# Kernel optimization log

Measured on AMD Instinct MI355X. Metric: run time of the kernel, lower is better.

## Reference

```python
import jax, jax.numpy as jnp
import numpy as np

DIM, HEADS, HD, WS, SHIFT = 768, 48, 16, 3, 1
EPS = 1e-5


def setup_inputs() -> dict:
    key = jax.random.key(0)
    ks = jax.random.split(key, 6)
    s = 0.02  # init scale for weights
    return {
        "x": jax.random.normal(ks[0], (8, 4096, DIM), jnp.float32),
        "g1": jnp.ones((DIM,), jnp.float32),
        "b1": jnp.zeros((DIM,), jnp.float32),
        "w_qkv": jax.random.normal(ks[1], (DIM, 3 * DIM), jnp.float32) * s,
        "w_proj": jax.random.normal(ks[2], (DIM, DIM), jnp.float32) * s,
        "g2": jnp.ones((DIM,), jnp.float32),
        "b2": jnp.zeros((DIM,), jnp.float32),
        "w_mlp1": jax.random.normal(ks[3], (DIM, 2 * DIM), jnp.float32) * s,
        "b_mlp1": jnp.zeros((2 * DIM,), jnp.float32),
        "w_mlp2": jax.random.normal(ks[4], (2 * DIM, DIM), jnp.float32) * s,
        "b_mlp2": jnp.zeros((DIM,), jnp.float32),
    }


def _ln(x, g, b):
    m = x.mean(-1, keepdims=True)
    v = ((x - m) ** 2).mean(-1, keepdims=True)
    return (x - m) * jax.lax.rsqrt(v + EPS) * g + b


def _shifted_window_attention(x, w_qkv, w_proj):
    B, T, C = x.shape
    pad_r = (WS - T % WS) % WS
    xp = jnp.pad(x, ((0, 0), (0, pad_r), (0, 0)))
    Tp = T + pad_r
    xs = jnp.roll(xp, -SHIFT, axis=1) if SHIFT > 0 else xp
    xw = xs.reshape(B, Tp // WS, WS, C)            # [B, nW, ws, C]
    qkv = (xw @ w_qkv).reshape(B, Tp // WS, WS, 3, HEADS, HD)
    q, k, v = jnp.moveaxis(qkv, 3, 0)              # each [B, nW, ws, H, hd]
    attn = jnp.einsum("bnihd,bnjhd->bnhij", q, k) * (HD ** -0.5)
    attn = jax.nn.softmax(attn, axis=-1)           # [B, nW, H, ws, ws]
    o = jnp.einsum("bnhij,bnjhd->bnihd", attn, v).reshape(B, Tp, C)
    o = o @ w_proj
    if SHIFT > 0:
        o = jnp.roll(o, SHIFT, axis=1)
    return o[:, :T]


def reference(x, g1, b1, w_qkv, w_proj, g2, b2, w_mlp1, b_mlp1, w_mlp2, b_mlp2):
    x = x + _shifted_window_attention(_ln(x, g1, b1), w_qkv, w_proj)
    h = _ln(x, g2, b2)
    x = x + (jax.nn.relu(h @ w_mlp1 + b_mlp1) @ w_mlp2 + b_mlp2)
    return x
```

## Files before the change

kernel.cpp:

```cpp
#include <hip/hip_runtime.h>

#define BATCH 8
#define TLEN  4096
#define DIM   768
#define TP    4098
#define NWIN  1366
#define HEADS 48
#define HD    16
#define MREAL (BATCH*TP)
#define MP    32896
#define M2    (BATCH*TLEN)

typedef unsigned short u16;
typedef __bf16  bf16x8  __attribute__((ext_vector_type(8)));
typedef short   short8v __attribute__((ext_vector_type(8)));
typedef float   float4v __attribute__((ext_vector_type(4)));
typedef u16     u16x4   __attribute__((ext_vector_type(4)));

static __device__ __forceinline__ float bf2f(u16 u) {
  unsigned int x = ((unsigned int)u) << 16;
  return __builtin_bit_cast(float, x);
}
static __device__ __forceinline__ u16 f2bf(float f) {
  unsigned int x = __builtin_bit_cast(unsigned int, f);
  x += 0x7fffu + ((x >> 16) & 1u);
  return (u16)(x >> 16);
}

static __device__ __forceinline__ float4v mfma_bf16(short8v a, short8v b, float4v c) {
  return __builtin_amdgcn_mfma_f32_16x16x32_bf16(
      __builtin_bit_cast(bf16x8, a), __builtin_bit_cast(bf16x8, b), c, 0, 0, 0);
}

static __device__ __forceinline__ void gload_lds16(const u16* src, u16* ldsdst) {
  __builtin_amdgcn_global_load_lds(
      (const __attribute__((address_space(1))) void*)src,
      (__attribute__((address_space(3))) void*)ldsdst,
      16, 0, 0);
}

__global__ __launch_bounds__(256) void cvt_transpose(const float* __restrict__ w,
                                                     u16* __restrict__ wt,
                                                     int K, int N) {
  int idx = blockIdx.x * 256 + threadIdx.x;
  if (idx >= K * N) return;
  int k = idx / N, n = idx - k * N;
  wt[(size_t)n * K + k] = f2bf(w[idx]);
}

template<bool ROLL>
__global__ __launch_bounds__(256) void ln_kernel(const float* __restrict__ x,
                                                 const float* __restrict__ g,
                                                 const float* __restrict__ bet,
                                                 u16* __restrict__ out) {
  int wave = threadIdx.x >> 6, lane = threadIdx.x & 63;
  int row = blockIdx.x * 4 + wave;
  u16* orow = out + (size_t)row * DIM;

  const float* src;
  if (ROLL) {
    bool zero = (row >= MREAL);
    int t = 0, b = 0;
    if (!zero) {
      b = row / TP;
      int m = row - b * TP;
      t = m + 1; if (t == TP) t = 0;
      if (t >= TLEN) zero = true;
    }
    if (zero) {
      u16x4 z = {};
#pragma unroll
      for (int c = 0; c < 3; ++c) *(u16x4*)&orow[c * 256 + lane * 4] = z;
      return;
    }
    src = x + ((size_t)b * TLEN + t) * DIM;
  } else {
    src = x + (size_t)row * DIM;
  }

  float v[12];
  float s = 0.f, s2 = 0.f;
#pragma unroll
  for (int c = 0; c < 3; ++c) {
    float4v f = *(const float4v*)&src[c * 256 + lane * 4];
#pragma unroll
    for (int q = 0; q < 4; ++q) { v[c * 4 + q] = f[q]; s += f[q]; s2 += f[q] * f[q]; }
  }
#pragma unroll
  for (int off = 1; off < 64; off <<= 1) {
    s  += __shfl_xor(s, off);
    s2 += __shfl_xor(s2, off);
  }
  float mean = s * (1.f / DIM);
  float var  = s2 * (1.f / DIM) - mean * mean;
  float rs   = rsqrtf(var + 1e-5f);
#pragma unroll
  for (int c = 0; c < 3; ++c) {
    int col = c * 256 + lane * 4;
    float4v gv = *(const float4v*)&g[col];
    float4v bv = *(const float4v*)&bet[col];
    u16x4 o4;
#pragma unroll
    for (int q = 0; q < 4; ++q) o4[q] = f2bf((v[c * 4 + q] - mean) * rs * gv[q] + bv[q]);
    *(u16x4*)&orow[col] = o4;
  }
}

__global__ __launch_bounds__(256) void lnb_kernel(const u16* __restrict__ xin,
                                                  const float* __restrict__ g,
                                                  const float* __restrict__ bet,
                                                  u16* __restrict__ out) {
  int wave = threadIdx.x >> 6, lane = threadIdx.x & 63;
  int row = blockIdx.x * 4 + wave;
  const u16* src = xin + (size_t)row * DIM;
  u16* orow = out + (size_t)row * DIM;

  float v[12];
  float s = 0.f, s2 = 0.f;
#pragma unroll
  for (int c = 0; c < 3; ++c) {
    u16x4 h = *(const u16x4*)&src[c * 256 + lane * 4];
#pragma unroll
    for (int q = 0; q < 4; ++q) {
      float f = bf2f(h[q]);
      v[c * 4 + q] = f; s += f; s2 += f * f;
    }
  }
#pragma unroll
  for (int off = 1; off < 64; off <<= 1) {
    s  += __shfl_xor(s, off);
    s2 += __shfl_xor(s2, off);
  }
  float mean = s * (1.f / DIM);
  float var  = s2 * (1.f / DIM) - mean * mean;
  float rs   = rsqrtf(var + 1e-5f);
#pragma unroll
  for (int c = 0; c < 3; ++c) {
    int col = c * 256 + lane * 4;
    float4v gv = *(const float4v*)&g[col];
    float4v bv = *(const float4v*)&bet[col];
    u16x4 o4;
#pragma unroll
    for (int q = 0; q < 4; ++q) o4[q] = f2bf((v[c * 4 + q] - mean) * rs * gv[q] + bv[q]);
    *(u16x4*)&orow[col] = o4;
  }
}

__global__ __launch_bounds__(256) void attn_kernel(const u16* __restrict__ qkv,
                                                   u16* __restrict__ o) {
  int gid = blockIdx.x * 256 + threadIdx.x;
  int h = gid % HEADS;
  int w = gid / HEADS;
  int b = w / NWIN, wl = w - b * NWIN;
  size_t row0 = (size_t)b * TP + (size_t)wl * 3;

  float q[3][HD], k[3][HD];
#pragma unroll
  for (int t = 0; t < 3; ++t) {
    const u16* rp = qkv + (row0 + t) * (3 * DIM) + h * HD;
    short8v q0 = *(const short8v*)(rp);
    short8v q1 = *(const short8v*)(rp + 8);
    short8v k0 = *(const short8v*)(rp + DIM);
    short8v k1 = *(const short8v*)(rp + DIM + 8);
#pragma unroll
    for (int d = 0; d < 8; ++d) {
      q[t][d] = bf2f((u16)q0[d]); q[t][d + 8] = bf2f((u16)q1[d]);
      k[t][d] = bf2f((u16)k0[d]); k[t][d + 8] = bf2f((u16)k1[d]);
    }
  }
  float p[3][3];
#pragma unroll
  for (int i = 0; i < 3; ++i)
#pragma unroll
    for (int j = 0; j < 3; ++j) {
      float s = 0.f;
#pragma unroll
      for (int d = 0; d < HD; ++d) s += q[i][d] * k[j][d];
      p[i][j] = s * 0.25f;
    }
#pragma unroll
  for (int i = 0; i < 3; ++i) {
    float mx = fmaxf(p[i][0], fmaxf(p[i][1], p[i][2]));
    float e0 = __expf(p[i][0] - mx), e1 = __expf(p[i][1] - mx), e2 = __expf(p[i][2] - mx);
    float inv = 1.f / (e0 + e1 + e2);
    p[i][0] = e0 * inv; p[i][1] = e1 * inv; p[i][2] = e2 * inv;
  }
  float acc[3][HD];
#pragma unroll
  for (int i = 0; i < 3; ++i)
#pragma unroll
    for (int d = 0; d < HD; ++d) acc[i][d] = 0.f;
#pragma unroll
  for (int t = 0; t < 3; ++t) {
    const u16* rp = qkv + (row0 + t) * (3 * DIM) + 2 * DIM + h * HD;
    short8v v0 = *(const short8v*)(rp);
    short8v v1 = *(const short8v*)(rp + 8);
#pragma unroll
    for (int d = 0; d < 8; ++d) {
      float a = bf2f((u16)v0[d]), bb = bf2f((u16)v1[d]);
#pragma unroll
      for (int i = 0; i < 3; ++i) { acc[i][d] += p[i][t] * a; acc[i][d + 8] += p[i][t] * bb; }
    }
  }
#pragma unroll
  for (int i = 0; i < 3; ++i) {
    u16 tmp[HD];
#pragma unroll
    for (int d = 0; d < HD; ++d) tmp[d] = f2bf(acc[i][d]);
    u16* op = o + (row0 + i) * DIM + h * HD;
    *(short8v*)op = *(short8v*)tmp;
    *(short8v*)(op + 8) = *(short8v*)(tmp + 8);
  }
}

template<int EPI>
__global__ __launch_bounds__(512, 6) void gemm8w(const u16* __restrict__ A,
                                                 const u16* __restrict__ Bt,
                                                 int N, int K,
                                                 u16* __restrict__ outb,
                                                 float* __restrict__ outf,
                                                 const float* __restrict__ residf,
                                                 const u16* __restrict__ residb,
                                                 const float* __restrict__ bias) {
  __shared__ u16 As[128 * 64];
  __shared__ u16 Bs[128 * 64];
  const int tid = threadIdx.x;
  const int wave = tid >> 6, lane = tid & 63;
  const int wm = wave >> 2, wn = wave & 3;
  const int r = lane & 15, gq = lane >> 4;

  const int nwg = gridDim.x, gx = N >> 7;
  int wg = blockIdx.x;
  int qd = nwg >> 3, rr = nwg & 7, xcd = wg & 7, lid = wg >> 3;
  int swz = (xcd < rr ? xcd * (qd + 1) : rr * (qd + 1) + (xcd - rr) * qd) + lid;
  const int tm = swz / gx, tn = swz - tm * gx;
  const int arow0 = tm * 128, brow0 = tn * 128;

  int srow[2], scol[2];
#pragma unroll
  for (int c = 0; c < 2; ++c) {
    int d = c * 8192 + tid * 16;
    srow[c] = d >> 7;
    scol[c] = (((d & 127) ^ ((srow[c] & 7) << 4)) >> 1);
  }

  const int kx0 = (((gq * 16) ^ ((r & 7) << 4)) >> 1);
  const int kx1 = (((64 + gq * 16) ^ ((r & 7) << 4)) >> 1);
  const int rA = wm * 64 + r, rB = wn * 32 + r;

  float4v acc[4][2];
#pragma unroll
  for (int i = 0; i < 4; ++i)
#pragma unroll
    for (int j = 0; j < 2; ++j) acc[i][j] = (float4v){0.f, 0.f, 0.f, 0.f};

  const int NT = K >> 6;
  for (int t = 0; t < NT; ++t) {
    const int k0 = t << 6;
#pragma unroll
    for (int c = 0; c < 2; ++c) {
      gload_lds16(A  + (size_t)(arow0 + srow[c]) * K + k0 + scol[c],
                  &As[0] + c * 4096 + tid * 8);
      gload_lds16(Bt + (size_t)(brow0 + srow[c]) * K + k0 + scol[c],
                  &Bs[0] + c * 4096 + tid * 8);
    }
    __syncthreads();
#pragma unroll
    for (int kk = 0; kk < 2; ++kk) {
      const int kx = kk ? kx1 : kx0;
      short8v af[4], bfr[2];
#pragma unroll
      for (int i = 0; i < 4; ++i)
        af[i] = *(const short8v*)&As[(rA + i * 16) * 64 + kx];
#pragma unroll
      for (int j = 0; j < 2; ++j)
        bfr[j] = *(const short8v*)&Bs[(rB + j * 16) * 64 + kx];
#pragma unroll
      for (int i = 0; i < 4; ++i)
#pragma unroll
        for (int j = 0; j < 2; ++j)
          acc[i][j] = mfma_bf16(af[i], bfr[j], acc[i][j]);
    }
    __syncthreads();
  }

#pragma unroll
  for (int i = 0; i < 4; ++i) {
#pragma unroll
    for (int j = 0; j < 2; ++j) {
      int colg = brow0 + wn * 32 + j * 16 + r;
      int rowb = arow0 + wm * 64 + i * 16 + gq * 4;
#pragma unroll
      for (int v = 0; v < 4; ++v) {
        int rg = rowb + v;
        float val = acc[i][j][v];
        if constexpr (EPI == 0) {
          outb[(size_t)rg * N + colg] = f2bf(val);
        } else if constexpr (EPI == 1) {
          if (rg < MREAL) {
            int b = rg / TP, m = rg - b * TP;
            int t = m + 1; if (t == TP) t = 0;
            if (t < TLEN) {
              size_t idx = ((size_t)b * TLEN + t) * DIM + colg;
              outb[idx] = f2bf(residf[idx] + val);
            }
          }
        } else if constexpr (EPI == 2) {
          float z = val + bias[colg];
          outb[(size_t)rg * N + colg] = f2bf(z > 0.f ? z : 0.f);
        } else {
          size_t idx = (size_t)rg * N + colg;
          outf[idx] = bf2f(residb[idx]) + val + bias[colg];
        }
      }
    }
  }
}

extern "C" void kernel_launch(void* const* d_in, const int* in_sizes, int n_in,
                              void* d_out, int out_size, void* d_ws, size_t ws_size,
                              hipStream_t stream) {
  const float* x      = (const float*)d_in[0];
  const float* g1     = (const float*)d_in[1];
  const float* b1     = (const float*)d_in[2];
  const float* w_qkv  = (const float*)d_in[3];
  const float* w_proj = (const float*)d_in[4];
  const float* g2     = (const float*)d_in[5];
  const float* b2     = (const float*)d_in[6];
  const float* w_mlp1 = (const float*)d_in[7];
  const float* b_mlp1 = (const float*)d_in[8];
  const float* w_mlp2 = (const float*)d_in[9];
  const float* b_mlp2 = (const float*)d_in[10];
  float* out = (float*)d_out;

  u16* xs     = (u16*)d_ws;
  u16* qkv    = xs     + (size_t)MP * DIM;
  u16* obuf   = qkv    + (size_t)MP * 3 * DIM;
  u16* wqkvT  = obuf   + (size_t)MP * DIM;
  u16* wprojT = wqkvT  + (size_t)3 * DIM * DIM;
  u16* wm1T   = wprojT + (size_t)DIM * DIM;
  u16* wm2T   = wm1T   + (size_t)2 * DIM * DIM;
  u16* resf = xs;
  u16* ln2o = obuf;
  u16* h1   = qkv;

  cvt_transpose<<<(DIM * 3 * DIM + 255) / 256, 256, 0, stream>>>(w_qkv,  wqkvT,  DIM,     3 * DIM);
  cvt_transpose<<<(DIM * DIM + 255)     / 256, 256, 0, stream>>>(w_proj, wprojT, DIM,     DIM);
  cvt_transpose<<<(DIM * 2 * DIM + 255) / 256, 256, 0, stream>>>(w_mlp1, wm1T,   DIM,     2 * DIM);
  cvt_transpose<<<(2 * DIM * DIM + 255) / 256, 256, 0, stream>>>(w_mlp2, wm2T,   2 * DIM, DIM);

  ln_kernel<true><<<MP / 4, 256, 0, stream>>>(x, g1, b1, xs);

  gemm8w<0><<<(MP / 128) * (3 * DIM / 128), 512, 0, stream>>>(
      xs, wqkvT, 3 * DIM, DIM, qkv, nullptr, nullptr, nullptr, nullptr);

  attn_kernel<<<(BATCH * NWIN * HEADS) / 256, 256, 0, stream>>>(qkv, obuf);

  gemm8w<1><<<(MP / 128) * (DIM / 128), 512, 0, stream>>>(
      obuf, wprojT, DIM, DIM, resf, nullptr, x, nullptr, nullptr);

  lnb_kernel<<<M2 / 4, 256, 0, stream>>>(resf, g2, b2, ln2o);

  gemm8w<2><<<(M2 / 128) * (2 * DIM / 128), 512, 0, stream>>>(
      ln2o, wm1T, 2 * DIM, DIM, h1, nullptr, nullptr, nullptr, b_mlp1);

  gemm8w<3><<<(M2 / 128) * (DIM / 128), 512, 0, stream>>>(
      h1, wm2T, DIM, 2 * DIM, nullptr, out, nullptr, resf, b_mlp2);
}
```

Measured before the change: 535.9 us.

## Double-buffer LDS tiles in gemm8w to overlap global loads with MFMA

Converts the GEMM main loop to a two-stage LDS ping-pong: the next K-tile is issued via direct-to-LDS loads before the current tile is consumed, with explicit vmcnt/lgkmcnt waits and barriers. All fragments are loaded into registers first, then a second barrier frees the buffer and the MFMAs run at raised wave priority. This is meant to hide global load latency behind compute. In exchange LDS use per block doubles and the occupancy hint drops from 6 to 4 blocks per CU.

```diff
diff --git a/kernel.cpp b/kernel.cpp
--- a/kernel.cpp
+++ b/kernel.cpp
@@ -214,7 +214,7 @@
 }
 
 template<int EPI>
-__global__ __launch_bounds__(512, 6) void gemm8w(const u16* __restrict__ A,
+__global__ __launch_bounds__(512, 4) void gemm8w(const u16* __restrict__ A,
                                                  const u16* __restrict__ Bt,
                                                  int N, int K,
                                                  u16* __restrict__ outb,
@@ -222,8 +222,8 @@
                                                  const float* __restrict__ residf,
                                                  const u16* __restrict__ residb,
                                                  const float* __restrict__ bias) {
-  __shared__ u16 As[128 * 64];
-  __shared__ u16 Bs[128 * 64];
+  __shared__ u16 As[2][128 * 64];
+  __shared__ u16 Bs[2][128 * 64];
   const int tid = threadIdx.x;
   const int wave = tid >> 6, lane = tid & 63;
   const int wm = wave >> 2, wn = wave & 3;
@@ -254,34 +254,54 @@
 #pragma unroll
     for (int j = 0; j < 2; ++j) acc[i][j] = (float4v){0.f, 0.f, 0.f, 0.f};
 
+  auto stage = [&](int buf, int tk) {
+#pragma unroll
+    for (int c = 0; c < 2; ++c) {
+      gload_lds16(A  + (size_t)(arow0 + srow[c]) * K + tk * 64 + scol[c],
+                  &As[buf][0] + c * 4096 + tid * 8);
+      gload_lds16(Bt + (size_t)(brow0 + srow[c]) * K + tk * 64 + scol[c],
+                  &Bs[buf][0] + c * 4096 + tid * 8);
+    }
+  };
+
   const int NT = K >> 6;
+  stage(0, 0);
   for (int t = 0; t < NT; ++t) {
-    const int k0 = t << 6;
-#pragma unroll
-    for (int c = 0; c < 2; ++c) {
-      gload_lds16(A  + (size_t)(arow0 + srow[c]) * K + k0 + scol[c],
-                  &As[0] + c * 4096 + tid * 8);
-      gload_lds16(Bt + (size_t)(brow0 + srow[c]) * K + k0 + scol[c],
-                  &Bs[0] + c * 4096 + tid * 8);
-    }
-    __syncthreads();
-#pragma unroll
-    for (int kk = 0; kk < 2; ++kk) {
-      const int kx = kk ? kx1 : kx0;
-      short8v af[4], bfr[2];
-#pragma unroll
-      for (int i = 0; i < 4; ++i)
-        af[i] = *(const short8v*)&As[(rA + i * 16) * 64 + kx];
-#pragma unroll
-      for (int j = 0; j < 2; ++j)
-        bfr[j] = *(const short8v*)&Bs[(rB + j * 16) * 64 + kx];
-#pragma unroll
-      for (int i = 0; i < 4; ++i)
-#pragma unroll
-        for (int j = 0; j < 2; ++j)
-          acc[i][j] = mfma_bf16(af[i], bfr[j], acc[i][j]);
-    }
-    __syncthreads();
+    const int cur = t & 1;
+    if (t + 1 < NT) {
+      stage(cur ^ 1, t + 1);
+      asm volatile("s_waitcnt vmcnt(4)" ::: "memory");
+    } else {
+      asm volatile("s_waitcnt vmcnt(0)" ::: "memory");
+    }
+    __builtin_amdgcn_sched_barrier(0);
+    __builtin_amdgcn_s_barrier();
+    __builtin_amdgcn_sched_barrier(0);
+
+    short8v af[8], bfr[4];
+#pragma unroll
+    for (int i = 0; i < 4; ++i) {
+      af[2 * i]     = *(const short8v*)&As[cur][(rA + i * 16) * 64 + kx0];
+      af[2 * i + 1] = *(const short8v*)&As[cur][(rA + i * 16) * 64 + kx1];
+    }
+#pragma unroll
+    for (int j = 0; j < 2; ++j) {
+      bfr[2 * j]     = *(const short8v*)&Bs[cur][(rB + j * 16) * 64 + kx0];
+      bfr[2 * j + 1] = *(const short8v*)&Bs[cur][(rB + j * 16) * 64 + kx1];
+    }
+    asm volatile("s_waitcnt lgkmcnt(0)" ::: "memory");
+    __builtin_amdgcn_sched_barrier(0);
+    __builtin_amdgcn_s_barrier();
+    __builtin_amdgcn_s_setprio(1);
+#pragma unroll
+    for (int i = 0; i < 4; ++i)
+#pragma unroll
+      for (int j = 0; j < 2; ++j) {
+        acc[i][j] = mfma_bf16(af[2 * i],     bfr[2 * j],     acc[i][j]);
+        acc[i][j] = mfma_bf16(af[2 * i + 1], bfr[2 * j + 1], acc[i][j]);
+      }
+    __builtin_amdgcn_s_setprio(0);
+    __builtin_amdgcn_sched_barrier(0);
   }
 
 #pragma unroll
```

After: 592.2 us. +10.5%, slower.
